# Kernel tuning notes

Measured on AMD Instinct MI355X. Metric: run time of the kernel, lower is better.

The kernel has to match this reference:

```python
import jax, jax.numpy as jnp
import numpy as np

# Dimensions (AlphaFold-scale IPA / GeometricFrameAttention)
B, N = 1, 768
C_S, C_Z, C_H, H, PQ, PV = 384, 128, 16, 12, 4, 8
INF = 1e9
EPS = 1e-8
SOFTPLUS_INV_1 = 0.541324854612918  # gfa_point_weights_init_


def quat_to_rot(q):
    """Unit-normalize quaternions [..., 4] -> rotation matrices [..., 3, 3]."""
    q = q / jnp.linalg.norm(q, axis=-1, keepdims=True)
    w, x, y, z = q[..., 0], q[..., 1], q[..., 2], q[..., 3]
    R = jnp.stack([
        1 - 2 * (y * y + z * z), 2 * (x * y - w * z), 2 * (x * z + w * y),
        2 * (x * y + w * z), 1 - 2 * (x * x + z * z), 2 * (y * z - w * x),
        2 * (x * z - w * y), 2 * (y * z + w * x), 1 - 2 * (x * x + y * y),
    ], axis=-1)
    return R.reshape(q.shape[:-1] + (3, 3))


def setup_inputs() -> dict:
    key = jax.random.key(0)
    ks = jax.random.split(key, 12)

    def lin(k, out_d, in_d):
        return jax.random.normal(k, (out_d, in_d), jnp.float32) * (1.0 / np.sqrt(in_d))

    out_in = H * C_H + H * PV * 4 + H * C_Z  # o + o_pt(x,y,z) + o_pt_norm + o_pair
    inp = {
        "s": jax.random.normal(ks[0], (B, N, C_S), jnp.float32),
        "z": jax.random.normal(ks[1], (B, N, N, C_Z), jnp.float32),
        "rot": quat_to_rot(jax.random.normal(ks[2], (B, N, 4), jnp.float32)),
        "trans": jax.random.normal(ks[3], (B, N, 3), jnp.float32),
        "mask": jnp.ones((B, N), jnp.float32),
        "Wq": lin(ks[4], H * C_H, C_S),
        "bq": jnp.zeros((H * C_H,), jnp.float32),
        "Wkv": lin(ks[5], H * 2 * C_H, C_S),
        "bkv": jnp.zeros((H * 2 * C_H,), jnp.float32),
        "Wqp": lin(ks[6], H * PQ * 3, C_S),
        "bqp": jnp.zeros((H * PQ * 3,), jnp.float32),
        "Wkvp": lin(ks[7], H * (PQ + PV) * 3, C_S),
        "bkvp": jnp.zeros((H * (PQ + PV) * 3,), jnp.float32),
        "Wb": lin(ks[8], H, C_Z),
        "bb": jnp.zeros((H,), jnp.float32),
        "head_w": jnp.full((H,), SOFTPLUS_INV_1, jnp.float32),
        "Wout": lin(ks[9], C_S, out_in),
        "bout": jnp.zeros((C_S,), jnp.float32),
    }
    return inp


def _forward(s, z, rot, trans, mask, Wq, bq, Wkv, bkv, Wqp, bqp, Wkvp, bkvp,
             Wb, bb, head_w, Wout, bout):
    Bn, Nn, _ = s.shape
    # scalar q/k/v
    q = (s @ Wq.T + bq).reshape(Bn, Nn, H, C_H)
    kv = (s @ Wkv.T + bkv).reshape(Bn, Nn, H, 2 * C_H)
    k, v = kv[..., :C_H], kv[..., C_H:]
    # point q/k/v: local frame -> global frame (x_glob = R x_loc + t)
    q_pts = (s @ Wqp.T + bqp).reshape(Bn, Nn, H * PQ, 3)
    q_pts = (jnp.einsum('bnxy,bnpy->bnpx', rot, q_pts) + trans[:, :, None]).reshape(Bn, Nn, H, PQ, 3)
    kv_pts = (s @ Wkvp.T + bkvp).reshape(Bn, Nn, H * (PQ + PV), 3)
    kv_pts = (jnp.einsum('bnxy,bnpy->bnpx', rot, kv_pts) + trans[:, :, None]).reshape(Bn, Nn, H, PQ + PV, 3)
    k_pts, v_pts = kv_pts[..., :PQ, :], kv_pts[..., PQ:, :]
    # pair bias [B,N,N,H] -> [B,H,N,N]
    bias = z @ Wb.T + bb
    a = jnp.einsum('bihc,bjhc->bhij', q, k) * np.float32(np.sqrt(1.0 / (3 * C_H)))
    a = a + np.float32(np.sqrt(1.0 / 3.0)) * jnp.transpose(bias, (0, 3, 1, 2))
    # point distance term: sum_p |q_p - k_p|^2 = |q|^2 + |k|^2 - 2 q.k (no [B,N,N,H,P,3] tensor)
    q2 = jnp.sum(q_pts ** 2, axis=(-1, -2))  # [B,N,H]
    k2 = jnp.sum(k_pts ** 2, axis=(-1, -2))
    qk = jnp.einsum('bihpc,bjhpc->bhij', q_pts, k_pts)
    d2 = q2.transpose(0, 2, 1)[..., :, None] + k2.transpose(0, 2, 1)[..., None, :] - 2.0 * qk
    hw = jax.nn.softplus(head_w) * np.float32(np.sqrt(2.0 / (27.0 * PQ)))  # sqrt(1/(3*(PQ*9/2)))
    a = a - 0.5 * hw[None, :, None, None] * d2
    # mask bias
    sq_mask = mask[..., :, None] * mask[..., None, :]
    a = a + (INF * (sq_mask - 1.0))[:, None]
    a = jax.nn.softmax(a, axis=-1)  # [B,H,N,N]
    # outputs
    o = jnp.einsum('bhij,bjhc->bihc', a, v).reshape(Bn, Nn, H * C_H)
    o_pt = jnp.einsum('bhij,bjhpc->bihpc', a, v_pts)  # global frame
    o_pt = jnp.einsum('bnyx,bnhpy->bnhpx', rot, o_pt - trans[:, :, None, None])  # back to local
    o_pt_norm = jnp.sqrt(jnp.sum(o_pt ** 2, axis=-1) + EPS).reshape(Bn, Nn, H * PV)
    o_pt_flat = jnp.moveaxis(o_pt, -1, -3).reshape(Bn, Nn, 3 * H * PV)  # coord-major like unbind+cat
    o_pair = jnp.einsum('bhij,bijc->bihc', a, z).reshape(Bn, Nn, H * C_Z)
    cat = jnp.concatenate([o, o_pt_flat, o_pt_norm, o_pair], axis=-1)
    return cat @ Wout.T + bout


def reference(s, z, rot, trans, mask, Wq, bq, Wkv, bkv, Wqp, bqp, Wkvp, bkvp,
              Wb, bb, head_w, Wout, bout):
    return _forward(s, z, rot, trans, mask, Wq, bq, Wkv, bkv, Wqp, bqp,
                    Wkvp, bkvp, Wb, bb, head_w, Wout, bout)
```

## Files before the change

kernel.cpp:

```cpp
#include <hip/hip_runtime.h>
#include <math.h>

#define NN 768
#define CS 384
#define CZ 128
#define CH 16
#define HH 12
#define PQ 4
#define PV 8
#define OUTIN 2112

#define SC_QK 0.14433756729740643f
#define SC_B  0.57735026918962576f
#define SC_HW 0.13608276348795434f
#define MSLACK 12.0f

__global__ __launch_bounds__(256) void kproj(
    const float* __restrict__ s,
    const float* __restrict__ Wq,  const float* __restrict__ bq,
    const float* __restrict__ Wkv, const float* __restrict__ bkv,
    const float* __restrict__ Wqp, const float* __restrict__ bqp,
    const float* __restrict__ Wkvp,const float* __restrict__ bkvp,
    float* __restrict__ q, float* __restrict__ kT, float* __restrict__ vallT,
    float* __restrict__ qpr, float* __restrict__ kvpr)
{
    __shared__ float s_lds[8*384];
    int n0 = blockIdx.x * 8;
    int t = threadIdx.x;
    for (int idx = t; idx < 8*384; idx += 256)
        s_lds[idx] = s[(n0 + idx/384)*384 + (idx%384)];
    __syncthreads();

    int o = blockIdx.y * 128 + (t & 127);
    int ng = t >> 7;
    const float* wrow; float bias;
    if (o < 192)      { wrow = Wq   + o*384;       bias = bq[o]; }
    else if (o < 576) { wrow = Wkv  + (o-192)*384; bias = bkv[o-192]; }
    else if (o < 720) { wrow = Wqp  + (o-576)*384; bias = bqp[o-576]; }
    else              { wrow = Wkvp + (o-720)*384; bias = bkvp[o-720]; }

    float acc[4] = {bias, bias, bias, bias};
    const float4* wr4 = reinterpret_cast<const float4*>(wrow);
    for (int c4 = 0; c4 < 96; ++c4) {
        float4 w = wr4[c4];
        #pragma unroll
        for (int nn = 0; nn < 4; ++nn) {
            const float* sr = &s_lds[(ng*4+nn)*384 + c4*4];
            acc[nn] = fmaf(w.x, sr[0], acc[nn]);
            acc[nn] = fmaf(w.y, sr[1], acc[nn]);
            acc[nn] = fmaf(w.z, sr[2], acc[nn]);
            acc[nn] = fmaf(w.w, sr[3], acc[nn]);
        }
    }
    #pragma unroll
    for (int nn = 0; nn < 4; ++nn) {
        int n = n0 + ng*4 + nn;
        float v = acc[nn];
        if (o < 192)      q[n*192 + o] = v;
        else if (o < 576) {
            int oo = o - 192, h = oo >> 5, cc = oo & 31;
            if (cc < 16) kT[(h*NN + n)*16 + cc] = v;
            else         vallT[(size_t)(h*40 + (cc-16))*NN + n] = v;
        }
        else if (o < 720) qpr[n*144 + (o-576)] = v;
        else              kvpr[n*432 + (o-720)] = v;
    }
}

__global__ __launch_bounds__(192) void krot(
    const float* __restrict__ rot, const float* __restrict__ trans,
    const float* __restrict__ qpr, const float* __restrict__ kvpr,
    float* __restrict__ qp, float* __restrict__ kpT, float* __restrict__ vallT)
{
    int n = blockIdx.x;
    __shared__ float R[9], T[3];
    int t = threadIdx.x;
    if (t < 9) R[t] = rot[n*9 + t];
    if (t < 3) T[t] = trans[n*3 + t];
    __syncthreads();

    const float* src = (t < 48) ? (qpr + n*144 + t*3) : (kvpr + n*432 + (t-48)*3);
    float x = src[0], y = src[1], z = src[2];
    float wx = R[0]*x + R[1]*y + R[2]*z + T[0];
    float wy = R[3]*x + R[4]*y + R[5]*z + T[1];
    float wz = R[6]*x + R[7]*y + R[8]*z + T[2];
    if (t < 48) {
        float* d = qp + n*144 + t*3;
        d[0]=wx; d[1]=wy; d[2]=wz;
    } else {
        int pi = t - 48, h = pi/12, pp = pi%12;
        if (pp < 4) {
            float* d = kpT + (h*NN+n)*12 + pp*3;
            d[0]=wx; d[1]=wy; d[2]=wz;
        } else {
            int ch = h*40 + 16 + (pp-4)*3;
            vallT[(size_t)(ch+0)*NN + n] = wx;
            vallT[(size_t)(ch+1)*NN + n] = wy;
            vallT[(size_t)(ch+2)*NN + n] = wz;
        }
    }
}

__global__ __launch_bounds__(256) void kqk(
    const float* __restrict__ kT, const float* __restrict__ kpT,
    const float* __restrict__ q, const float* __restrict__ qp,
    const float* __restrict__ mask, const float* __restrict__ head_w,
    const float* __restrict__ bb, float* __restrict__ lqd,
    float* __restrict__ mpart)
{
    const int j0 = blockIdx.x * 64;
    const int i0 = blockIdx.y * 32;
    __shared__ float ktl[64][17], kpl[64][13];
    __shared__ float ql[32][17],  qpl[32][13];
    __shared__ float mi_l[32], mj_l[64];
    __shared__ float mpl[32][12];
    const int t = threadIdx.x;
    if (t < 32) mi_l[t] = mask[i0 + t];
    if (t < 64) mj_l[t] = mask[j0 + t];

    const int jl = t & 63, wv = t >> 6;

    for (int h = 0; h < 12; ++h) {
        __syncthreads();
        for (int idx = t; idx < 1024; idx += 256)
            ktl[idx >> 4][idx & 15] = kT[(size_t)(h*NN + j0 + (idx >> 4))*16 + (idx & 15)];
        for (int idx = t; idx < 768; idx += 256) {
            int r = idx / 12, e = idx - r*12;
            kpl[r][e] = kpT[(size_t)(h*NN + j0 + r)*12 + e];
        }
        for (int idx = t; idx < 512; idx += 256)
            ql[idx >> 4][idx & 15] = q[(i0 + (idx >> 4))*192 + h*16 + (idx & 15)];
        for (int idx = t; idx < 384; idx += 256) {
            int r = idx / 12, e = idx - r*12;
            qpl[r][e] = qp[(i0 + r)*144 + h*12 + e];
        }
        __syncthreads();

        const float hwh = log1pf(expf(head_w[h])) * SC_HW;
        const float bbh = bb[h] * SC_B;
        const float mj = mj_l[jl];
        #pragma unroll
        for (int k = 0; k < 8; ++k) {
            const int il = wv*8 + k;
            float qk = 0.f;
            #pragma unroll
            for (int c = 0; c < 16; ++c) qk = fmaf(ktl[jl][c], ql[il][c], qk);
            float d2 = 0.f;
            #pragma unroll
            for (int e = 0; e < 12; ++e) { float d = qpl[il][e] - kpl[jl][e]; d2 = fmaf(d, d, d2); }
            float mt = 1e9f * (mi_l[il]*mj - 1.0f);
            float lg = fmaf(qk, SC_QK, fmaf(-0.5f*hwh, d2, bbh)) + mt;
            lqd[((size_t)(i0+il)*NN + j0 + jl)*12 + h] = lg;
            float m = lg;
            m = fmaxf(m, __shfl_xor(m, 1, 64));
            m = fmaxf(m, __shfl_xor(m, 2, 64));
            m = fmaxf(m, __shfl_xor(m, 4, 64));
            m = fmaxf(m, __shfl_xor(m, 8, 64));
            m = fmaxf(m, __shfl_xor(m, 16, 64));
            m = fmaxf(m, __shfl_xor(m, 32, 64));
            if (jl == 0) mpl[il][h] = m;
        }
    }
    __syncthreads();
    if (t < 384) {
        int il = t / 12, h = t - il*12;
        mpart[((size_t)h*NN + i0 + il)*12 + blockIdx.x] = mpl[il][h];
    }
}

__global__ __launch_bounds__(256, 6) void kpexp(
    const float* __restrict__ z, const float* __restrict__ Wb,
    const float* __restrict__ mpart, float* __restrict__ p_io,
    float* __restrict__ ssum)
{
    __shared__ float M_lds[12];
    __shared__ float sred[4][12];
    const int i = blockIdx.x, jseg = blockIdx.y;
    const int t = threadIdx.x, w = t >> 6, l = t & 63;
    if (t < 12) {
        const float4* mp = (const float4*)(mpart + ((size_t)t*NN + i)*12);
        float4 a = mp[0], b = mp[1], c = mp[2];
        float m = fmaxf(fmaxf(fmaxf(a.x,a.y), fmaxf(a.z,a.w)),
                 fmaxf(fmaxf(fmaxf(b.x,b.y), fmaxf(b.z,b.w)),
                       fmaxf(fmaxf(c.x,c.y), fmaxf(c.z,c.w))));
        M_lds[t] = m + MSLACK;
    }
    __syncthreads();

    const int j = jseg*256 + t;
    const float4* __restrict__ zr4 = (const float4*)(z + ((size_t)i*NN + j)*CZ);
    const float4* __restrict__ wb4 = (const float4*)Wb;

    float b0=0,b1=0,b2=0,b3=0,b4=0,b5=0,b6=0,b7=0,b8=0,b9=0,b10=0,b11=0;
    #define HD(B, H) { float4 wv = wb4[(H)*32 + c4]; \
        B = fmaf(zv.x, wv.x, B); B = fmaf(zv.y, wv.y, B); \
        B = fmaf(zv.z, wv.z, B); B = fmaf(zv.w, wv.w, B); }
    #pragma unroll 4
    for (int c4 = 0; c4 < 32; ++c4) {
        float4 zv = zr4[c4];
        HD(b0,0) HD(b1,1) HD(b2,2)  HD(b3,3)  HD(b4,4)   HD(b5,5)
        HD(b6,6) HD(b7,7) HD(b8,8)  HD(b9,9)  HD(b10,10) HD(b11,11)
    }
    #undef HD

    float* gp = p_io + ((size_t)i*NN + j)*12;
    float4 qa = *(const float4*)(gp + 0);
    float4 qb = *(const float4*)(gp + 4);
    float4 qc = *(const float4*)(gp + 8);
    float p0  = __expf(fmaf(b0,  SC_B, qa.x) - M_lds[0]);
    float p1  = __expf(fmaf(b1,  SC_B, qa.y) - M_lds[1]);
    float p2  = __expf(fmaf(b2,  SC_B, qa.z) - M_lds[2]);
    float p3  = __expf(fmaf(b3,  SC_B, qa.w) - M_lds[3]);
    float p4  = __expf(fmaf(b4,  SC_B, qb.x) - M_lds[4]);
    float p5  = __expf(fmaf(b5,  SC_B, qb.y) - M_lds[5]);
    float p6  = __expf(fmaf(b6,  SC_B, qb.z) - M_lds[6]);
    float p7  = __expf(fmaf(b7,  SC_B, qb.w) - M_lds[7]);
    float p8  = __expf(fmaf(b8,  SC_B, qc.x) - M_lds[8]);
    float p9  = __expf(fmaf(b9,  SC_B, qc.y) - M_lds[9]);
    float p10 = __expf(fmaf(b10, SC_B, qc.z) - M_lds[10]);
    float p11 = __expf(fmaf(b11, SC_B, qc.w) - M_lds[11]);
    float4 oa; oa.x = p0; oa.y = p1;  oa.z = p2;  oa.w = p3;
    float4 ob; ob.x = p4; ob.y = p5;  ob.z = p6;  ob.w = p7;
    float4 oc; oc.x = p8; oc.y = p9;  oc.z = p10; oc.w = p11;
    *(float4*)(gp + 0) = oa;
    *(float4*)(gp + 4) = ob;
    *(float4*)(gp + 8) = oc;

    #define RED(P) { P += __shfl_xor(P, 1, 64);  P += __shfl_xor(P, 2, 64); \
                     P += __shfl_xor(P, 4, 64);  P += __shfl_xor(P, 8, 64); \
                     P += __shfl_xor(P, 16, 64); P += __shfl_xor(P, 32, 64); }
    RED(p0) RED(p1) RED(p2) RED(p3) RED(p4)  RED(p5)
    RED(p6) RED(p7) RED(p8) RED(p9) RED(p10) RED(p11)
    #undef RED
    if (l == 0) {
        sred[w][0] = p0; sred[w][1] = p1; sred[w][2]  = p2;  sred[w][3]  = p3;
        sred[w][4] = p4; sred[w][5] = p5; sred[w][6]  = p6;  sred[w][7]  = p7;
        sred[w][8] = p8; sred[w][9] = p9; sred[w][10] = p10; sred[w][11] = p11;
    }
    __syncthreads();
    if (t < 12)
        ssum[(size_t)jseg*(12*NN) + t*NN + i] =
            sred[0][t] + sred[1][t] + sred[2][t] + sred[3][t];
}

__global__ __launch_bounds__(256, 3) void kfin(
    const float* __restrict__ z, const float* __restrict__ vallT,
    const float* __restrict__ p, const float* __restrict__ ssum,
    const float* __restrict__ rot, const float* __restrict__ trans,
    float* __restrict__ cat)
{
    __shared__ float an_l[12][776];
    __shared__ float4 psum[2][12][16];
    __shared__ float sinv[12];
    __shared__ float optl[12][24];
    __shared__ float R[9], T[3];
    const int i = blockIdx.x, jh = blockIdx.y;
    const int t = threadIdx.x, w = t >> 6, l = t & 63;
    if (t < 9) R[t] = rot[i*9 + t];
    if (t < 3) T[t] = trans[i*3 + t];
    if (t >= 16 && t < 28) {
        const int h = t - 16;
        sinv[h] = 1.0f / (ssum[h*NN + i] + ssum[12*NN + h*NN + i] + ssum[24*NN + h*NN + i]);
    }

    const float4* pr4 = (const float4*)(p + (size_t)i*NN*12);
    #pragma unroll
    for (int jj = 0; jj < 3; ++jj) {
        const int j = jj*256 + t;
        float4 ga = pr4[j*3 + 0];
        float4 gb = pr4[j*3 + 1];
        float4 gc = pr4[j*3 + 2];
        an_l[0][j] = ga.x;  an_l[1][j] = ga.y;  an_l[2][j]  = ga.z;  an_l[3][j]  = ga.w;
        an_l[4][j] = gb.x;  an_l[5][j] = gb.y;  an_l[6][j]  = gb.z;  an_l[7][j]  = gb.w;
        an_l[8][j] = gc.x;  an_l[9][j] = gc.y;  an_l[10][j] = gc.z;  an_l[11][j] = gc.w;
    }
    __syncthreads();

    {
        const int hgrp = w & 1, jseg = w >> 1;
        const int h0 = hgrp*6;
        const int jo = l >> 4, c4b = l & 15;
        const float4* __restrict__ zr = (const float4*)(z + (size_t)i*NN*CZ) + jh*16 + c4b;
        float4 a0 = {0,0,0,0}, a1 = {0,0,0,0}, a2 = {0,0,0,0};
        float4 a3 = {0,0,0,0}, a4 = {0,0,0,0}, a5 = {0,0,0,0};
        for (int jb = 0; jb < 24; ++jb) {
            const int j0 = jseg*384 + jb*16 + jo*4;
            float4 z0 = zr[(size_t)(j0+0)*32];
            float4 z1 = zr[(size_t)(j0+1)*32];
            float4 z2 = zr[(size_t)(j0+2)*32];
            float4 z3 = zr[(size_t)(j0+3)*32];
            #define PBH(A, HH) { \
                float4 pv = *(const float4*)&an_l[h0+(HH)][j0]; \
                A.x = fmaf(pv.x, z0.x, A.x); A.y = fmaf(pv.x, z0.y, A.y); \
                A.z = fmaf(pv.x, z0.z, A.z); A.w = fmaf(pv.x, z0.w, A.w); \
                A.x = fmaf(pv.y, z1.x, A.x); A.y = fmaf(pv.y, z1.y, A.y); \
                A.z = fmaf(pv.y, z1.z, A.z); A.w = fmaf(pv.y, z1.w, A.w); \
                A.x = fmaf(pv.z, z2.x, A.x); A.y = fmaf(pv.z, z2.y, A.y); \
                A.z = fmaf(pv.z, z2.z, A.z); A.w = fmaf(pv.z, z2.w, A.w); \
                A.x = fmaf(pv.w, z3.x, A.x); A.y = fmaf(pv.w, z3.y, A.y); \
                A.z = fmaf(pv.w, z3.z, A.z); A.w = fmaf(pv.w, z3.w, A.w); }
            PBH(a0,0) PBH(a1,1) PBH(a2,2) PBH(a3,3) PBH(a4,4) PBH(a5,5)
            #undef PBH
        }
        #define FOLD(V) \
            V.x += __shfl_xor(V.x, 16, 64); V.y += __shfl_xor(V.y, 16, 64); \
            V.z += __shfl_xor(V.z, 16, 64); V.w += __shfl_xor(V.w, 16, 64); \
            V.x += __shfl_xor(V.x, 32, 64); V.y += __shfl_xor(V.y, 32, 64); \
            V.z += __shfl_xor(V.z, 32, 64); V.w += __shfl_xor(V.w, 32, 64);
        FOLD(a0) FOLD(a1) FOLD(a2) FOLD(a3) FOLD(a4) FOLD(a5)
        #undef FOLD
        if (l < 16) {
            psum[jseg][h0+0][c4b] = a0;
            psum[jseg][h0+1][c4b] = a1;
            psum[jseg][h0+2][c4b] = a2;
            psum[jseg][h0+3][c4b] = a3;
            psum[jseg][h0+4][c4b] = a4;
            psum[jseg][h0+5][c4b] = a5;
        }
    }
    __syncthreads();
    if (t < 192) {
        const int hh = t >> 4, cc = t & 15;
        float4 v0 = psum[0][hh][cc], v1 = psum[1][hh][cc];
        const float sc = sinv[hh];
        float4 o;
        o.x = (v0.x + v1.x) * sc;
        o.y = (v0.y + v1.y) * sc;
        o.z = (v0.z + v1.z) * sc;
        o.w = (v0.w + v1.w) * sc;
        *(float4*)(cat + (size_t)i*OUTIN + 576 + hh*128 + jh*64 + cc*4) = o;
    }

    if (jh == 0) return;

    float* crow = cat + (size_t)i*OUTIN;
    for (int cc = 0; cc < 120; ++cc) {
        const int ch = w*120 + cc;
        const int h = ch / 40, e = ch % 40;
        const float2* __restrict__ vr = (const float2*)(vallT + (size_t)ch*NN);
        const float2* __restrict__ pr = (const float2*)(&an_l[h][0]);
        float ax = 0.f, ay = 0.f;
        #pragma unroll
        for (int jc = 0; jc < 6; ++jc) {
            float2 v = vr[jc*64 + l];
            float2 pp = pr[jc*64 + l];
            ax = fmaf(pp.x, v.x, ax);
            ay = fmaf(pp.y, v.y, ay);
        }
        float sv = ax + ay;
        #pragma unroll
        for (int off = 32; off >= 1; off >>= 1) sv += __shfl_xor(sv, off, 64);
        if (l == 0) {
            float val = sv * sinv[h];
            if (e < 16) crow[h*16 + e] = val;
            else        optl[h][e-16] = val;
        }
    }
    __syncthreads();
    if (t < 96) {
        int h = t >> 3, pp = t & 7;
        float wx = optl[h][pp*3+0] - T[0];
        float wy = optl[h][pp*3+1] - T[1];
        float wz = optl[h][pp*3+2] - T[2];
        crow[192 + 0*96 + h*8 + pp] = R[0]*wx + R[3]*wy + R[6]*wz;
        crow[192 + 1*96 + h*8 + pp] = R[1]*wx + R[4]*wy + R[7]*wz;
        crow[192 + 2*96 + h*8 + pp] = R[2]*wx + R[5]*wy + R[8]*wz;
        crow[480 + h*8 + pp] = sqrtf(fmaf(wx,wx,fmaf(wy,wy,wz*wz)) + 1e-8f);
    }
}

__global__ __launch_bounds__(256) void koutp(
    const float* __restrict__ cat, const float* __restrict__ Wout,
    float* __restrict__ ptmp)
{
    __shared__ float ct[32][36];
    __shared__ float wt[64][36];
    const int n0 = blockIdx.x * 32, o0 = blockIdx.y * 64;
    const int k0 = blockIdx.z * 352;
    const int t = threadIdx.x;
    const int tn = (t >> 4) * 2;
    const int to = t & 15;

    float a00=0,a01=0,a02=0,a03=0, a10=0,a11=0,a12=0,a13=0;

    for (int c = 0; c < 11; ++c) {
        __syncthreads();
        #pragma unroll
        for (int u = 0; u < 4; ++u) {
            int idx = u*256 + t, r = idx >> 5, cc = idx & 31;
            ct[r][cc] = cat[(size_t)(n0 + r)*OUTIN + k0 + c*32 + cc];
        }
        #pragma unroll
        for (int u = 0; u < 8; ++u) {
            int idx = u*256 + t, r = idx >> 5, cc = idx & 31;
            wt[r][cc] = Wout[(size_t)(o0 + r)*OUTIN + k0 + c*32 + cc];
        }
        __syncthreads();
        #pragma unroll
        for (int kk = 0; kk < 32; kk += 4) {
            float4 c0 = *(const float4*)&ct[tn][kk];
            float4 c1 = *(const float4*)&ct[tn+1][kk];
            float4 w0 = *(const float4*)&wt[to][kk];
            float4 w1 = *(const float4*)&wt[to+16][kk];
            float4 w2 = *(const float4*)&wt[to+32][kk];
            float4 w3 = *(const float4*)&wt[to+48][kk];
            a00 = fmaf(c0.x,w0.x,a00); a00 = fmaf(c0.y,w0.y,a00); a00 = fmaf(c0.z,w0.z,a00); a00 = fmaf(c0.w,w0.w,a00);
            a01 = fmaf(c0.x,w1.x,a01); a01 = fmaf(c0.y,w1.y,a01); a01 = fmaf(c0.z,w1.z,a01); a01 = fmaf(c0.w,w1.w,a01);
            a02 = fmaf(c0.x,w2.x,a02); a02 = fmaf(c0.y,w2.y,a02); a02 = fmaf(c0.z,w2.z,a02); a02 = fmaf(c0.w,w2.w,a02);
            a03 = fmaf(c0.x,w3.x,a03); a03 = fmaf(c0.y,w3.y,a03); a03 = fmaf(c0.z,w3.z,a03); a03 = fmaf(c0.w,w3.w,a03);
            a10 = fmaf(c1.x,w0.x,a10); a10 = fmaf(c1.y,w0.y,a10); a10 = fmaf(c1.z,w0.z,a10); a10 = fmaf(c1.w,w0.w,a10);
            a11 = fmaf(c1.x,w1.x,a11); a11 = fmaf(c1.y,w1.y,a11); a11 = fmaf(c1.z,w1.z,a11); a11 = fmaf(c1.w,w1.w,a11);
            a12 = fmaf(c1.x,w2.x,a12); a12 = fmaf(c1.y,w2.y,a12); a12 = fmaf(c1.z,w2.z,a12); a12 = fmaf(c1.w,w2.w,a12);
            a13 = fmaf(c1.x,w3.x,a13); a13 = fmaf(c1.y,w3.y,a13); a13 = fmaf(c1.z,w3.z,a13); a13 = fmaf(c1.w,w3.w,a13);
        }
    }
    float* pb = ptmp + (size_t)blockIdx.z * (NN*384);
    pb[(size_t)(n0+tn+0)*384 + o0+to+ 0] = a00;
    pb[(size_t)(n0+tn+0)*384 + o0+to+16] = a01;
    pb[(size_t)(n0+tn+0)*384 + o0+to+32] = a02;
    pb[(size_t)(n0+tn+0)*384 + o0+to+48] = a03;
    pb[(size_t)(n0+tn+1)*384 + o0+to+ 0] = a10;
    pb[(size_t)(n0+tn+1)*384 + o0+to+16] = a11;
    pb[(size_t)(n0+tn+1)*384 + o0+to+32] = a12;
    pb[(size_t)(n0+tn+1)*384 + o0+to+48] = a13;
}

__global__ __launch_bounds__(256) void kred(
    const float* __restrict__ ptmp, const float* __restrict__ bout,
    float* __restrict__ out)
{
    int idx = blockIdx.x * 256 + threadIdx.x;
    int o = idx % 384;
    float v = bout[o];
    #pragma unroll
    for (int s = 0; s < 6; ++s) v += ptmp[(size_t)s*(NN*384) + idx];
    out[idx] = v;
}

extern "C" void kernel_launch(void* const* d_in, const int* in_sizes, int n_in,
                              void* d_out, int out_size, void* d_ws, size_t ws_size,
                              hipStream_t stream) {
    const float* s      = (const float*)d_in[0];
    const float* z      = (const float*)d_in[1];
    const float* rot    = (const float*)d_in[2];
    const float* trans  = (const float*)d_in[3];
    const float* mask   = (const float*)d_in[4];
    const float* Wq     = (const float*)d_in[5];
    const float* bq     = (const float*)d_in[6];
    const float* Wkv    = (const float*)d_in[7];
    const float* bkv    = (const float*)d_in[8];
    const float* Wqp    = (const float*)d_in[9];
    const float* bqp    = (const float*)d_in[10];
    const float* Wkvp   = (const float*)d_in[11];
    const float* bkvp   = (const float*)d_in[12];
    const float* Wb     = (const float*)d_in[13];
    const float* bb     = (const float*)d_in[14];
    const float* head_w = (const float*)d_in[15];
    const float* Wout   = (const float*)d_in[16];
    const float* bout   = (const float*)d_in[17];
    float* out = (float*)d_out;
    float* ws  = (float*)d_ws;

    float* q     = ws;
    float* kT    = ws + 147456;
    float* kpT   = ws + 294912;
    float* vallT = ws + 405504;
    float* qp    = ws + 774144;
    float* qpr   = ws + 884736;
    float* kvpr  = ws + 995328;
    float* mpart = ws + 1327104;
    float* ssum  = ws + 1437696;
    float* cat   = ws + 1465344;
    float* lqd   = ws + 3087360;
    float* ptmp  = ws + 10165248;

    kproj<<<dim3(96, 9), 256, 0, stream>>>(s, Wq, bq, Wkv, bkv, Wqp, bqp, Wkvp, bkvp,
                                           q, kT, vallT, qpr, kvpr);
    krot<<<dim3(768), 192, 0, stream>>>(rot, trans, qpr, kvpr, qp, kpT, vallT);
    kqk<<<dim3(12, 24), 256, 0, stream>>>(kT, kpT, q, qp, mask, head_w, bb, lqd, mpart);
    kpexp<<<dim3(768, 3), 256, 0, stream>>>(z, Wb, mpart, lqd, ssum);
    kfin<<<dim3(768, 2), 256, 0, stream>>>(z, vallT, lqd, ssum, rot, trans, cat);
    koutp<<<dim3(24, 6, 6), 256, 0, stream>>>(cat, Wout, ptmp);
    kred<<<dim3(1152), 256, 0, stream>>>(ptmp, bout, out);
}
```

Baseline: 472.0 us.

## Split finalize kernel into separate pair-bias and value/point kernels

Splits the combined finalize kernel into two. kfinB computes o_pair directly from global probabilities and z without staging in shared memory, over a 768x4 grid with all 12 heads per thread. kfinC handles the value and point outputs with no LDS staging of the pair path and launch bounds raised to 4 blocks per SM. The aim is to raise occupancy and parallelism for the z-streaming reduction and to stop the jh==0 blocks from idling. The cost is an extra kernel launch and re-reading probabilities from global memory in both kernels.

```diff
diff --git a/kernel.cpp b/kernel.cpp
--- a/kernel.cpp
+++ b/kernel.cpp
@@ -243,18 +243,84 @@
             sred[0][t] + sred[1][t] + sred[2][t] + sred[3][t];
 }
 
-__global__ __launch_bounds__(256, 3) void kfin(
-    const float* __restrict__ z, const float* __restrict__ vallT,
-    const float* __restrict__ p, const float* __restrict__ ssum,
+__global__ __launch_bounds__(256) void kfinB(
+    const float* __restrict__ z, const float* __restrict__ p,
+    const float* __restrict__ ssum, float* __restrict__ cat)
+{
+    __shared__ float4 opart[4][12][8];
+    __shared__ float sinv[12];
+    const int i = blockIdx.x, qq = blockIdx.y;
+    const int t = threadIdx.x, w = t >> 6, l = t & 63;
+    const int jo = l >> 3, c4 = l & 7;
+    if (t < 12)
+        sinv[t] = 1.0f / (ssum[t*NN + i] + ssum[12*NN + t*NN + i] + ssum[24*NN + t*NN + i]);
+
+    float4 a0={0,0,0,0},a1={0,0,0,0},a2={0,0,0,0},a3={0,0,0,0};
+    float4 a4={0,0,0,0},a5={0,0,0,0},a6={0,0,0,0},a7={0,0,0,0};
+    float4 a8={0,0,0,0},a9={0,0,0,0},a10={0,0,0,0},a11={0,0,0,0};
+
+    const float4* __restrict__ zb = (const float4*)(z + (size_t)i*NN*CZ) + qq*8 + c4;
+    const float4* __restrict__ pb = (const float4*)(p + (size_t)i*NN*12);
+
+    #pragma unroll 2
+    for (int jb = 0; jb < 24; ++jb) {
+        const int j = w*192 + jb*8 + jo;
+        float4 zv = zb[(size_t)j*32];
+        float4 pa = pb[j*3 + 0];
+        float4 pc = pb[j*3 + 1];
+        float4 pe = pb[j*3 + 2];
+        #define ACC(A, PS) { A.x = fmaf(PS, zv.x, A.x); A.y = fmaf(PS, zv.y, A.y); \
+                             A.z = fmaf(PS, zv.z, A.z); A.w = fmaf(PS, zv.w, A.w); }
+        ACC(a0, pa.x) ACC(a1, pa.y) ACC(a2,  pa.z) ACC(a3,  pa.w)
+        ACC(a4, pc.x) ACC(a5, pc.y) ACC(a6,  pc.z) ACC(a7,  pc.w)
+        ACC(a8, pe.x) ACC(a9, pe.y) ACC(a10, pe.z) ACC(a11, pe.w)
+        #undef ACC
+    }
+
+    #define FOLD(V) { \
+        V.x += __shfl_xor(V.x, 8, 64);  V.y += __shfl_xor(V.y, 8, 64);  \
+        V.z += __shfl_xor(V.z, 8, 64);  V.w += __shfl_xor(V.w, 8, 64);  \
+        V.x += __shfl_xor(V.x, 16, 64); V.y += __shfl_xor(V.y, 16, 64); \
+        V.z += __shfl_xor(V.z, 16, 64); V.w += __shfl_xor(V.w, 16, 64); \
+        V.x += __shfl_xor(V.x, 32, 64); V.y += __shfl_xor(V.y, 32, 64); \
+        V.z += __shfl_xor(V.z, 32, 64); V.w += __shfl_xor(V.w, 32, 64); }
+    FOLD(a0) FOLD(a1) FOLD(a2) FOLD(a3) FOLD(a4) FOLD(a5)
+    FOLD(a6) FOLD(a7) FOLD(a8) FOLD(a9) FOLD(a10) FOLD(a11)
+    #undef FOLD
+    if (jo == 0) {
+        opart[w][0][c4] = a0;   opart[w][1][c4] = a1;
+        opart[w][2][c4] = a2;   opart[w][3][c4] = a3;
+        opart[w][4][c4] = a4;   opart[w][5][c4] = a5;
+        opart[w][6][c4] = a6;   opart[w][7][c4] = a7;
+        opart[w][8][c4] = a8;   opart[w][9][c4] = a9;
+        opart[w][10][c4] = a10; opart[w][11][c4] = a11;
+    }
+    __syncthreads();
+    if (t < 96) {
+        const int h = t >> 3, cc = t & 7;
+        float4 v0 = opart[0][h][cc], v1 = opart[1][h][cc];
+        float4 v2 = opart[2][h][cc], v3 = opart[3][h][cc];
+        const float sc = sinv[h];
+        float4 o;
+        o.x = (v0.x + v1.x + v2.x + v3.x) * sc;
+        o.y = (v0.y + v1.y + v2.y + v3.y) * sc;
+        o.z = (v0.z + v1.z + v2.z + v3.z) * sc;
+        o.w = (v0.w + v1.w + v2.w + v3.w) * sc;
+        *(float4*)(cat + (size_t)i*OUTIN + 576 + h*128 + qq*32 + cc*4) = o;
+    }
+}
+
+__global__ __launch_bounds__(256, 4) void kfinC(
+    const float* __restrict__ vallT, const float* __restrict__ p,
+    const float* __restrict__ ssum,
     const float* __restrict__ rot, const float* __restrict__ trans,
     float* __restrict__ cat)
 {
     __shared__ float an_l[12][776];
-    __shared__ float4 psum[2][12][16];
     __shared__ float sinv[12];
     __shared__ float optl[12][24];
     __shared__ float R[9], T[3];
-    const int i = blockIdx.x, jh = blockIdx.y;
+    const int i = blockIdx.x;
     const int t = threadIdx.x, w = t >> 6, l = t & 63;
     if (t < 9) R[t] = rot[i*9 + t];
     if (t < 3) T[t] = trans[i*3 + t];
@@ -275,63 +341,6 @@
         an_l[8][j] = gc.x;  an_l[9][j] = gc.y;  an_l[10][j] = gc.z;  an_l[11][j] = gc.w;
     }
     __syncthreads();
-
-    {
-        const int hgrp = w & 1, jseg = w >> 1;
-        const int h0 = hgrp*6;
-        const int jo = l >> 4, c4b = l & 15;
-        const float4* __restrict__ zr = (const float4*)(z + (size_t)i*NN*CZ) + jh*16 + c4b;
-        float4 a0 = {0,0,0,0}, a1 = {0,0,0,0}, a2 = {0,0,0,0};
-        float4 a3 = {0,0,0,0}, a4 = {0,0,0,0}, a5 = {0,0,0,0};
-        for (int jb = 0; jb < 24; ++jb) {
-            const int j0 = jseg*384 + jb*16 + jo*4;
-            float4 z0 = zr[(size_t)(j0+0)*32];
-            float4 z1 = zr[(size_t)(j0+1)*32];
-            float4 z2 = zr[(size_t)(j0+2)*32];
-            float4 z3 = zr[(size_t)(j0+3)*32];
-            #define PBH(A, HH) { \
-                float4 pv = *(const float4*)&an_l[h0+(HH)][j0]; \
-                A.x = fmaf(pv.x, z0.x, A.x); A.y = fmaf(pv.x, z0.y, A.y); \
-                A.z = fmaf(pv.x, z0.z, A.z); A.w = fmaf(pv.x, z0.w, A.w); \
-                A.x = fmaf(pv.y, z1.x, A.x); A.y = fmaf(pv.y, z1.y, A.y); \
-                A.z = fmaf(pv.y, z1.z, A.z); A.w = fmaf(pv.y, z1.w, A.w); \
-                A.x = fmaf(pv.z, z2.x, A.x); A.y = fmaf(pv.z, z2.y, A.y); \
-                A.z = fmaf(pv.z, z2.z, A.z); A.w = fmaf(pv.z, z2.w, A.w); \
-                A.x = fmaf(pv.w, z3.x, A.x); A.y = fmaf(pv.w, z3.y, A.y); \
-                A.z = fmaf(pv.w, z3.z, A.z); A.w = fmaf(pv.w, z3.w, A.w); }
-            PBH(a0,0) PBH(a1,1) PBH(a2,2) PBH(a3,3) PBH(a4,4) PBH(a5,5)
-            #undef PBH
-        }
-        #define FOLD(V) \
-            V.x += __shfl_xor(V.x, 16, 64); V.y += __shfl_xor(V.y, 16, 64); \
-            V.z += __shfl_xor(V.z, 16, 64); V.w += __shfl_xor(V.w, 16, 64); \
-            V.x += __shfl_xor(V.x, 32, 64); V.y += __shfl_xor(V.y, 32, 64); \
-            V.z += __shfl_xor(V.z, 32, 64); V.w += __shfl_xor(V.w, 32, 64);
-        FOLD(a0) FOLD(a1) FOLD(a2) FOLD(a3) FOLD(a4) FOLD(a5)
-        #undef FOLD
-        if (l < 16) {
-            psum[jseg][h0+0][c4b] = a0;
-            psum[jseg][h0+1][c4b] = a1;
-            psum[jseg][h0+2][c4b] = a2;
-            psum[jseg][h0+3][c4b] = a3;
-            psum[jseg][h0+4][c4b] = a4;
-            psum[jseg][h0+5][c4b] = a5;
-        }
-    }
-    __syncthreads();
-    if (t < 192) {
-        const int hh = t >> 4, cc = t & 15;
-        float4 v0 = psum[0][hh][cc], v1 = psum[1][hh][cc];
-        const float sc = sinv[hh];
-        float4 o;
-        o.x = (v0.x + v1.x) * sc;
-        o.y = (v0.y + v1.y) * sc;
-        o.z = (v0.z + v1.z) * sc;
-        o.w = (v0.w + v1.w) * sc;
-        *(float4*)(cat + (size_t)i*OUTIN + 576 + hh*128 + jh*64 + cc*4) = o;
-    }
-
-    if (jh == 0) return;
 
     float* crow = cat + (size_t)i*OUTIN;
     for (int cc = 0; cc < 120; ++cc) {
@@ -479,7 +488,8 @@
     krot<<<dim3(768), 192, 0, stream>>>(rot, trans, qpr, kvpr, qp, kpT, vallT);
     kqk<<<dim3(12, 24), 256, 0, stream>>>(kT, kpT, q, qp, mask, head_w, bb, lqd, mpart);
     kpexp<<<dim3(768, 3), 256, 0, stream>>>(z, Wb, mpart, lqd, ssum);
-    kfin<<<dim3(768, 2), 256, 0, stream>>>(z, vallT, lqd, ssum, rot, trans, cat);
+    kfinB<<<dim3(768, 4), 256, 0, stream>>>(z, lqd, ssum, cat);
+    kfinC<<<dim3(768), 256, 0, stream>>>(vallT, lqd, ssum, rot, trans, cat);
     koutp<<<dim3(24, 6, 6), 256, 0, stream>>>(cat, Wout, ptmp);
     kred<<<dim3(1152), 256, 0, stream>>>(ptmp, bout, out);
 }
```

Result: slower. 493.0 us (+4.5%).

## Fuse pair-bias softmax exponent with attention-weighted z and v reductions

Applied to the files above, without the earlier changes.

The separate kpexp (bias + exp, writing probabilities back to memory) and kfin (re-reading z and probabilities for a·z and a·v) kernels are merged into one kernel. It computes the pair bias per 64-column tile, keeps the exponentials in LDS, and immediately accumulates them against z and the value rows. This is meant to avoid the probability round trip and make z effectively streamed once, with the second pass hitting cache. The value tensor layout changes from channel-major to row-major to suit the new access pattern. A small epilogue kernel then combines the two j-halves, normalizes, and applies the inverse frame. The cost is extra partial-sum buffers and heavy shuffle reductions in the bias step.

```diff
diff --git a/kernel.cpp b/kernel.cpp
--- a/kernel.cpp
+++ b/kernel.cpp
@@ -21,7 +21,7 @@
     const float* __restrict__ Wkv, const float* __restrict__ bkv,
     const float* __restrict__ Wqp, const float* __restrict__ bqp,
     const float* __restrict__ Wkvp,const float* __restrict__ bkvp,
-    float* __restrict__ q, float* __restrict__ kT, float* __restrict__ vallT,
+    float* __restrict__ q, float* __restrict__ kT, float* __restrict__ vall,
     float* __restrict__ qpr, float* __restrict__ kvpr)
 {
     __shared__ float s_lds[8*384];
@@ -60,7 +60,7 @@
         else if (o < 576) {
             int oo = o - 192, h = oo >> 5, cc = oo & 31;
             if (cc < 16) kT[(h*NN + n)*16 + cc] = v;
-            else         vallT[(size_t)(h*40 + (cc-16))*NN + n] = v;
+            else         vall[(size_t)n*480 + h*40 + (cc-16)] = v;
         }
         else if (o < 720) qpr[n*144 + (o-576)] = v;
         else              kvpr[n*432 + (o-720)] = v;
@@ -70,7 +70,7 @@
 __global__ __launch_bounds__(192) void krot(
     const float* __restrict__ rot, const float* __restrict__ trans,
     const float* __restrict__ qpr, const float* __restrict__ kvpr,
-    float* __restrict__ qp, float* __restrict__ kpT, float* __restrict__ vallT)
+    float* __restrict__ qp, float* __restrict__ kpT, float* __restrict__ vall)
 {
     int n = blockIdx.x;
     __shared__ float R[9], T[3];
@@ -93,10 +93,8 @@
             float* d = kpT + (h*NN+n)*12 + pp*3;
             d[0]=wx; d[1]=wy; d[2]=wz;
         } else {
-            int ch = h*40 + 16 + (pp-4)*3;
-            vallT[(size_t)(ch+0)*NN + n] = wx;
-            vallT[(size_t)(ch+1)*NN + n] = wy;
-            vallT[(size_t)(ch+2)*NN + n] = wz;
+            float* d = vall + (size_t)n*480 + h*40 + 16 + (pp-4)*3;
+            d[0]=wx; d[1]=wy; d[2]=wz;
         }
     }
 }
@@ -168,15 +166,22 @@
     }
 }
 
-__global__ __launch_bounds__(256, 6) void kpexp(
+__global__ __launch_bounds__(256) void kfuse(
     const float* __restrict__ z, const float* __restrict__ Wb,
-    const float* __restrict__ mpart, float* __restrict__ p_io,
-    float* __restrict__ ssum)
-{
-    __shared__ float M_lds[12];
-    __shared__ float sred[4][12];
+    const float* __restrict__ lqd, const float* __restrict__ mpart,
+    const float* __restrict__ vall,
+    float* __restrict__ opart, float* __restrict__ vpart, float* __restrict__ ssum)
+{
+    __shared__ float  M_lds[12];
+    __shared__ float  p_lds[12][66];
+    __shared__ float2 ofold[4][12][64];
+    __shared__ float  sredL[16][6];
+
     const int i = blockIdx.x, jseg = blockIdx.y;
     const int t = threadIdx.x, w = t >> 6, l = t & 63;
+    const int gid = t >> 4, cl = t & 15;
+    const int hhalf = gid & 1, h0 = hhalf * 6, jofs = gid >> 1;
+
     if (t < 12) {
         const float4* mp = (const float4*)(mpart + ((size_t)t*NN + i)*12);
         float4 a = mp[0], b = mp[1], c = mp[2];
@@ -185,176 +190,167 @@
                        fmaxf(fmaxf(c.x,c.y), fmaxf(c.z,c.w))));
         M_lds[t] = m + MSLACK;
     }
-    __syncthreads();
-
-    const int j = jseg*256 + t;
-    const float4* __restrict__ zr4 = (const float4*)(z + ((size_t)i*NN + j)*CZ);
-    const float4* __restrict__ wb4 = (const float4*)Wb;
-
-    float b0=0,b1=0,b2=0,b3=0,b4=0,b5=0,b6=0,b7=0,b8=0,b9=0,b10=0,b11=0;
-    #define HD(B, H) { float4 wv = wb4[(H)*32 + c4]; \
-        B = fmaf(zv.x, wv.x, B); B = fmaf(zv.y, wv.y, B); \
-        B = fmaf(zv.z, wv.z, B); B = fmaf(zv.w, wv.w, B); }
-    #pragma unroll 4
-    for (int c4 = 0; c4 < 32; ++c4) {
-        float4 zv = zr4[c4];
-        HD(b0,0) HD(b1,1) HD(b2,2)  HD(b3,3)  HD(b4,4)   HD(b5,5)
-        HD(b6,6) HD(b7,7) HD(b8,8)  HD(b9,9)  HD(b10,10) HD(b11,11)
-    }
-    #undef HD
-
-    float* gp = p_io + ((size_t)i*NN + j)*12;
-    float4 qa = *(const float4*)(gp + 0);
-    float4 qb = *(const float4*)(gp + 4);
-    float4 qc = *(const float4*)(gp + 8);
-    float p0  = __expf(fmaf(b0,  SC_B, qa.x) - M_lds[0]);
-    float p1  = __expf(fmaf(b1,  SC_B, qa.y) - M_lds[1]);
-    float p2  = __expf(fmaf(b2,  SC_B, qa.z) - M_lds[2]);
-    float p3  = __expf(fmaf(b3,  SC_B, qa.w) - M_lds[3]);
-    float p4  = __expf(fmaf(b4,  SC_B, qb.x) - M_lds[4]);
-    float p5  = __expf(fmaf(b5,  SC_B, qb.y) - M_lds[5]);
-    float p6  = __expf(fmaf(b6,  SC_B, qb.z) - M_lds[6]);
-    float p7  = __expf(fmaf(b7,  SC_B, qb.w) - M_lds[7]);
-    float p8  = __expf(fmaf(b8,  SC_B, qc.x) - M_lds[8]);
-    float p9  = __expf(fmaf(b9,  SC_B, qc.y) - M_lds[9]);
-    float p10 = __expf(fmaf(b10, SC_B, qc.z) - M_lds[10]);
-    float p11 = __expf(fmaf(b11, SC_B, qc.w) - M_lds[11]);
-    float4 oa; oa.x = p0; oa.y = p1;  oa.z = p2;  oa.w = p3;
-    float4 ob; ob.x = p4; ob.y = p5;  ob.z = p6;  ob.w = p7;
-    float4 oc; oc.x = p8; oc.y = p9;  oc.z = p10; oc.w = p11;
-    *(float4*)(gp + 0) = oa;
-    *(float4*)(gp + 4) = ob;
-    *(float4*)(gp + 8) = oc;
-
-    #define RED(P) { P += __shfl_xor(P, 1, 64);  P += __shfl_xor(P, 2, 64); \
-                     P += __shfl_xor(P, 4, 64);  P += __shfl_xor(P, 8, 64); \
-                     P += __shfl_xor(P, 16, 64); P += __shfl_xor(P, 32, 64); }
-    RED(p0) RED(p1) RED(p2) RED(p3) RED(p4)  RED(p5)
-    RED(p6) RED(p7) RED(p8) RED(p9) RED(p10) RED(p11)
-    #undef RED
-    if (l == 0) {
-        sred[w][0] = p0; sred[w][1] = p1; sred[w][2]  = p2;  sred[w][3]  = p3;
-        sred[w][4] = p4; sred[w][5] = p5; sred[w][6]  = p6;  sred[w][7]  = p7;
-        sred[w][8] = p8; sred[w][9] = p9; sred[w][10] = p10; sred[w][11] = p11;
-    }
-    __syncthreads();
-    if (t < 12)
-        ssum[(size_t)jseg*(12*NN) + t*NN + i] =
-            sred[0][t] + sred[1][t] + sred[2][t] + sred[3][t];
-}
-
-__global__ __launch_bounds__(256, 3) void kfin(
-    const float* __restrict__ z, const float* __restrict__ vallT,
-    const float* __restrict__ p, const float* __restrict__ ssum,
-    const float* __restrict__ rot, const float* __restrict__ trans,
-    float* __restrict__ cat)
-{
-    __shared__ float an_l[12][776];
-    __shared__ float4 psum[2][12][16];
+
+    float4 wva[6], wvb[6];
+    #pragma unroll
+    for (int h = 0; h < 6; ++h) {
+        const float4* wp = (const float4*)(Wb + (h0+h)*CZ + cl*8);
+        wva[h] = wp[0]; wvb[h] = wp[1];
+    }
+
+    float2 oa[12];
+    #pragma unroll
+    for (int h = 0; h < 12; ++h) { oa[h].x = 0.f; oa[h].y = 0.f; }
+    float2 vacc; vacc.x = 0.f; vacc.y = 0.f;
+    const int vch = 2*t;
+    const int vh  = (t < 240) ? (vch / 40) : 0;
+    float s_acc = 0.f;
+
+    __syncthreads();
+    const float Mh = M_lds[h0 + (cl < 6 ? cl : 5)];
+    const int jbase = jseg * 384;
+
+    for (int tile = 0; tile < 6; ++tile) {
+        const int jt = jbase + tile*64;
+
+        {
+            const float4* zq0 = (const float4*)(z + ((size_t)i*NN + jt + jofs)*CZ) + cl*2;
+            float4 za = zq0[0], zb = zq0[1];
+            for (int it = 0; it < 8; ++it) {
+                float4 zaN = za, zbN = zb;
+                if (it + 1 < 8) {
+                    const float4* zq = (const float4*)(z + ((size_t)i*NN + jt + (it+1)*8 + jofs)*CZ) + cl*2;
+                    zaN = zq[0]; zbN = zq[1];
+                }
+                const int j = jt + it*8 + jofs;
+                float b0, b1, b2, b3, b4, b5;
+                #define BDOT(BV, H)                                \
+                    BV = za.x*wva[H].x;                            \
+                    BV = fmaf(za.y, wva[H].y, BV);                 \
+                    BV = fmaf(za.z, wva[H].z, BV);                 \
+                    BV = fmaf(za.w, wva[H].w, BV);                 \
+                    BV = fmaf(zb.x, wvb[H].x, BV);                 \
+                    BV = fmaf(zb.y, wvb[H].y, BV);                 \
+                    BV = fmaf(zb.z, wvb[H].z, BV);                 \
+                    BV = fmaf(zb.w, wvb[H].w, BV);
+                BDOT(b0, 0) BDOT(b1, 1) BDOT(b2, 2) BDOT(b3, 3) BDOT(b4, 4) BDOT(b5, 5)
+                #undef BDOT
+                #define BRED(BV)                                   \
+                    BV += __shfl_xor(BV, 1, 16);                   \
+                    BV += __shfl_xor(BV, 2, 16);                   \
+                    BV += __shfl_xor(BV, 4, 16);                   \
+                    BV += __shfl_xor(BV, 8, 16);
+                BRED(b0) BRED(b1) BRED(b2) BRED(b3) BRED(b4) BRED(b5)
+                #undef BRED
+                float bsel = b0;
+                bsel = (cl == 1) ? b1 : bsel;
+                bsel = (cl == 2) ? b2 : bsel;
+                bsel = (cl == 3) ? b3 : bsel;
+                bsel = (cl == 4) ? b4 : bsel;
+                bsel = (cl == 5) ? b5 : bsel;
+                if (cl < 6) {
+                    float g = fmaf(bsel, SC_B, lqd[((size_t)i*NN + j)*12 + h0 + cl]);
+                    float p = __expf(g - Mh);
+                    p_lds[h0 + cl][j - jt] = p;
+                    s_acc += p;
+                }
+                za = zaN; zb = zbN;
+            }
+        }
+        __syncthreads();
+
+        {
+            const float2* zr2 = (const float2*)(z + (size_t)i*NN*CZ) + l;
+            #pragma unroll 4
+            for (int jj = 0; jj < 16; ++jj) {
+                const int jb = jj*4 + w;
+                float2 zv = zr2[(size_t)(jt + jb)*64];
+                #pragma unroll
+                for (int h = 0; h < 12; ++h) {
+                    float pv = p_lds[h][jb];
+                    oa[h].x = fmaf(pv, zv.x, oa[h].x);
+                    oa[h].y = fmaf(pv, zv.y, oa[h].y);
+                }
+            }
+        }
+
+        if (t < 240) {
+            const float2* vr = (const float2*)(vall + (size_t)jt*480 + vch);
+            #pragma unroll 4
+            for (int jb = 0; jb < 64; ++jb) {
+                float2 vv = vr[(size_t)jb*240];
+                float pv = p_lds[vh][jb];
+                vacc.x = fmaf(pv, vv.x, vacc.x);
+                vacc.y = fmaf(pv, vv.y, vacc.y);
+            }
+        }
+        __syncthreads();
+    }
+
+    #pragma unroll
+    for (int h = 0; h < 12; ++h) ofold[w][h][l] = oa[h];
+    if (cl < 6) sredL[gid][cl] = s_acc;
+    if (t < 240)
+        *((float2*)(vpart + ((size_t)(jseg*NN + i))*480) + t) = vacc;
+    __syncthreads();
+
+    float2* opw = (float2*)(opart + ((size_t)(jseg*NN + i))*1536);
+    #pragma unroll
+    for (int k = 0; k < 3; ++k) {
+        int slot = k*256 + t;
+        int h = slot >> 6, c2 = slot & 63;
+        float2 v0 = ofold[0][h][c2], v1 = ofold[1][h][c2];
+        float2 v2 = ofold[2][h][c2], v3 = ofold[3][h][c2];
+        float2 o;
+        o.x = v0.x + v1.x + v2.x + v3.x;
+        o.y = v0.y + v1.y + v2.y + v3.y;
+        opw[slot] = o;
+    }
+    if (t < 12) {
+        float sv = 0.f;
+        #pragma unroll
+        for (int k = 0; k < 8; ++k) sv += sredL[k*2 + (t/6)][t % 6];
+        ssum[(size_t)(jseg*12 + t)*NN + i] = sv;
+    }
+}
+
+__global__ __launch_bounds__(256) void kepi(
+    const float* __restrict__ opart, const float* __restrict__ vpart,
+    const float* __restrict__ ssum, const float* __restrict__ rot,
+    const float* __restrict__ trans, float* __restrict__ cat)
+{
     __shared__ float sinv[12];
     __shared__ float optl[12][24];
     __shared__ float R[9], T[3];
-    const int i = blockIdx.x, jh = blockIdx.y;
-    const int t = threadIdx.x, w = t >> 6, l = t & 63;
+    const int i = blockIdx.x, t = threadIdx.x;
     if (t < 9) R[t] = rot[i*9 + t];
     if (t < 3) T[t] = trans[i*3 + t];
     if (t >= 16 && t < 28) {
-        const int h = t - 16;
-        sinv[h] = 1.0f / (ssum[h*NN + i] + ssum[12*NN + h*NN + i] + ssum[24*NN + h*NN + i]);
-    }
-
-    const float4* pr4 = (const float4*)(p + (size_t)i*NN*12);
-    #pragma unroll
-    for (int jj = 0; jj < 3; ++jj) {
-        const int j = jj*256 + t;
-        float4 ga = pr4[j*3 + 0];
-        float4 gb = pr4[j*3 + 1];
-        float4 gc = pr4[j*3 + 2];
-        an_l[0][j] = ga.x;  an_l[1][j] = ga.y;  an_l[2][j]  = ga.z;  an_l[3][j]  = ga.w;
-        an_l[4][j] = gb.x;  an_l[5][j] = gb.y;  an_l[6][j]  = gb.z;  an_l[7][j]  = gb.w;
-        an_l[8][j] = gc.x;  an_l[9][j] = gc.y;  an_l[10][j] = gc.z;  an_l[11][j] = gc.w;
-    }
-    __syncthreads();
-
-    {
-        const int hgrp = w & 1, jseg = w >> 1;
-        const int h0 = hgrp*6;
-        const int jo = l >> 4, c4b = l & 15;
-        const float4* __restrict__ zr = (const float4*)(z + (size_t)i*NN*CZ) + jh*16 + c4b;
-        float4 a0 = {0,0,0,0}, a1 = {0,0,0,0}, a2 = {0,0,0,0};
-        float4 a3 = {0,0,0,0}, a4 = {0,0,0,0}, a5 = {0,0,0,0};
-        for (int jb = 0; jb < 24; ++jb) {
-            const int j0 = jseg*384 + jb*16 + jo*4;
-            float4 z0 = zr[(size_t)(j0+0)*32];
-            float4 z1 = zr[(size_t)(j0+1)*32];
-            float4 z2 = zr[(size_t)(j0+2)*32];
-            float4 z3 = zr[(size_t)(j0+3)*32];
-            #define PBH(A, HH) { \
-                float4 pv = *(const float4*)&an_l[h0+(HH)][j0]; \
-                A.x = fmaf(pv.x, z0.x, A.x); A.y = fmaf(pv.x, z0.y, A.y); \
-                A.z = fmaf(pv.x, z0.z, A.z); A.w = fmaf(pv.x, z0.w, A.w); \
-                A.x = fmaf(pv.y, z1.x, A.x); A.y = fmaf(pv.y, z1.y, A.y); \
-                A.z = fmaf(pv.y, z1.z, A.z); A.w = fmaf(pv.y, z1.w, A.w); \
-                A.x = fmaf(pv.z, z2.x, A.x); A.y = fmaf(pv.z, z2.y, A.y); \
-                A.z = fmaf(pv.z, z2.z, A.z); A.w = fmaf(pv.z, z2.w, A.w); \
-                A.x = fmaf(pv.w, z3.x, A.x); A.y = fmaf(pv.w, z3.y, A.y); \
-                A.z = fmaf(pv.w, z3.z, A.z); A.w = fmaf(pv.w, z3.w, A.w); }
-            PBH(a0,0) PBH(a1,1) PBH(a2,2) PBH(a3,3) PBH(a4,4) PBH(a5,5)
-            #undef PBH
-        }
-        #define FOLD(V) \
-            V.x += __shfl_xor(V.x, 16, 64); V.y += __shfl_xor(V.y, 16, 64); \
-            V.z += __shfl_xor(V.z, 16, 64); V.w += __shfl_xor(V.w, 16, 64); \
-            V.x += __shfl_xor(V.x, 32, 64); V.y += __shfl_xor(V.y, 32, 64); \
-            V.z += __shfl_xor(V.z, 32, 64); V.w += __shfl_xor(V.w, 32, 64);
-        FOLD(a0) FOLD(a1) FOLD(a2) FOLD(a3) FOLD(a4) FOLD(a5)
-        #undef FOLD
-        if (l < 16) {
-            psum[jseg][h0+0][c4b] = a0;
-            psum[jseg][h0+1][c4b] = a1;
-            psum[jseg][h0+2][c4b] = a2;
-            psum[jseg][h0+3][c4b] = a3;
-            psum[jseg][h0+4][c4b] = a4;
-            psum[jseg][h0+5][c4b] = a5;
-        }
-    }
-    __syncthreads();
-    if (t < 192) {
-        const int hh = t >> 4, cc = t & 15;
-        float4 v0 = psum[0][hh][cc], v1 = psum[1][hh][cc];
-        const float sc = sinv[hh];
-        float4 o;
-        o.x = (v0.x + v1.x) * sc;
-        o.y = (v0.y + v1.y) * sc;
-        o.z = (v0.z + v1.z) * sc;
-        o.w = (v0.w + v1.w) * sc;
-        *(float4*)(cat + (size_t)i*OUTIN + 576 + hh*128 + jh*64 + cc*4) = o;
-    }
-
-    if (jh == 0) return;
+        int h = t - 16;
+        sinv[h] = 1.0f / (ssum[(size_t)h*NN + i] + ssum[(size_t)(12+h)*NN + i]);
+    }
+    __syncthreads();
 
     float* crow = cat + (size_t)i*OUTIN;
-    for (int cc = 0; cc < 120; ++cc) {
-        const int ch = w*120 + cc;
-        const int h = ch / 40, e = ch % 40;
-        const float2* __restrict__ vr = (const float2*)(vallT + (size_t)ch*NN);
-        const float2* __restrict__ pr = (const float2*)(&an_l[h][0]);
-        float ax = 0.f, ay = 0.f;
-        #pragma unroll
-        for (int jc = 0; jc < 6; ++jc) {
-            float2 v = vr[jc*64 + l];
-            float2 pp = pr[jc*64 + l];
-            ax = fmaf(pp.x, v.x, ax);
-            ay = fmaf(pp.y, v.y, ay);
-        }
-        float sv = ax + ay;
-        #pragma unroll
-        for (int off = 32; off >= 1; off >>= 1) sv += __shfl_xor(sv, off, 64);
-        if (l == 0) {
-            float val = sv * sinv[h];
-            if (e < 16) crow[h*16 + e] = val;
-            else        optl[h][e-16] = val;
-        }
+    const float2* op0 = (const float2*)(opart + (size_t)i*1536);
+    const float2* op1 = (const float2*)(opart + (size_t)(NN + i)*1536);
+    #pragma unroll
+    for (int k = 0; k < 3; ++k) {
+        int slot = k*256 + t;
+        int h = slot >> 6, c2 = slot & 63;
+        float2 a = op0[slot], b = op1[slot];
+        float sc = sinv[h];
+        float2 o; o.x = (a.x + b.x)*sc; o.y = (a.y + b.y)*sc;
+        *(float2*)(crow + 576 + h*128 + c2*2) = o;
+    }
+    if (t < 240) {
+        const int ch = 2*t, h = ch/40, e = ch%40;
+        float2 v0 = *(const float2*)(vpart + (size_t)i*480 + ch);
+        float2 v1 = *(const float2*)(vpart + (size_t)(NN + i)*480 + ch);
+        float sc = sinv[h];
+        float vx = (v0.x + v1.x)*sc, vy = (v0.y + v1.y)*sc;
+        if (e < 16) { crow[h*16 + e] = vx; crow[h*16 + e + 1] = vy; }
+        else        { optl[h][e-16] = vx; optl[h][e-15] = vy; }
     }
     __syncthreads();
     if (t < 96) {
@@ -464,22 +460,24 @@
     float* q     = ws;
     float* kT    = ws + 147456;
     float* kpT   = ws + 294912;
-    float* vallT = ws + 405504;
+    float* vall  = ws + 405504;
     float* qp    = ws + 774144;
     float* qpr   = ws + 884736;
     float* kvpr  = ws + 995328;
     float* mpart = ws + 1327104;
     float* ssum  = ws + 1437696;
-    float* cat   = ws + 1465344;
-    float* lqd   = ws + 3087360;
-    float* ptmp  = ws + 10165248;
+    float* cat   = ws + 1456128;
+    float* lqd   = ws + 3078144;
+    float* opart = ws + 10156032;
+    float* vpart = ws + 12515328;
+    float* ptmp  = ws + 13252608;
 
     kproj<<<dim3(96, 9), 256, 0, stream>>>(s, Wq, bq, Wkv, bkv, Wqp, bqp, Wkvp, bkvp,
-                                           q, kT, vallT, qpr, kvpr);
-    krot<<<dim3(768), 192, 0, stream>>>(rot, trans, qpr, kvpr, qp, kpT, vallT);
+                                           q, kT, vall, qpr, kvpr);
+    krot<<<dim3(768), 192, 0, stream>>>(rot, trans, qpr, kvpr, qp, kpT, vall);
     kqk<<<dim3(12, 24), 256, 0, stream>>>(kT, kpT, q, qp, mask, head_w, bb, lqd, mpart);
-    kpexp<<<dim3(768, 3), 256, 0, stream>>>(z, Wb, mpart, lqd, ssum);
-    kfin<<<dim3(768, 2), 256, 0, stream>>>(z, vallT, lqd, ssum, rot, trans, cat);
+    kfuse<<<dim3(768, 2), 256, 0, stream>>>(z, Wb, lqd, mpart, vall, opart, vpart, ssum);
+    kepi<<<dim3(768), 256, 0, stream>>>(opart, vpart, ssum, rot, trans, cat);
     koutp<<<dim3(24, 6, 6), 256, 0, stream>>>(cat, Wout, ptmp);
     kred<<<dim3(1152), 256, 0, stream>>>(ptmp, bout, out);
 }
```

New measurement: 424.1 us. 10.1% less time.
